# Performance work log

Measured on AMD Instinct MI355X. Metric: run time of the kernel, lower is better.

Reference implementation:

```python
import jax, jax.numpy as jnp
import numpy as np

B, N, C, K = 8, 4096, 128, 20  # batch, points-per-cloud, channels (n_cout), knn neighbors
NEG_SLOPE = 0.01  # torch F.leaky_relu default


def setup_inputs() -> dict:
    key = jax.random.key(0)
    ks = jax.random.split(key, 6)
    s = 1.0 / np.sqrt(C).astype(np.float32)
    xyz = jax.random.normal(ks[0], (B, 3, N), jnp.float32)
    points = jax.random.normal(ks[1], (B, C, N), jnp.float32)
    Wc = jax.random.normal(ks[2], (C, C), jnp.float32) * s  # center 1x1 conv weight (out,in)
    bc = jax.random.normal(ks[3], (C,), jnp.float32) * s
    Wg = jax.random.normal(ks[4], (C, C), jnp.float32) * s  # grouped 1x1 conv weight
    bg = jax.random.normal(ks[5], (C,), jnp.float32) * s
    return {"xyz": xyz, "points": points, "Wc": Wc, "bc": bc, "Wg": Wg, "bg": bg}


def reference(xyz, points, Wc, bc, Wg, bg):
    # xyz: [B,3,N], points: [B,C,N]
    k = K
    shortcut = points
    p = jax.nn.leaky_relu(points, NEG_SLOPE)        # [B,C,N]
    pt = jnp.transpose(p, (0, 2, 1))                # [B,N,C]
    xt = jnp.transpose(xyz, (0, 2, 1))              # [B,N,3]

    # pairwise squared distances [B,N,N]
    sq_norm = jnp.sum(xt * xt, axis=-1)             # [B,N]
    sq = sq_norm[:, :, None] - 2.0 * jnp.einsum('bnd,bmd->bnm', xt, xt) + sq_norm[:, None, :]

    # knn: k+1 nearest (incl. self), drop self -> [B,N,k]
    _, idx = jax.lax.top_k(-sq, k + 1)
    idx = idx[:, :, 1:]

    # gather neighbor features: [B,N,k,C]
    grouped = jax.vmap(lambda a, i: a[i])(pt, idx)

    # center 1x1 conv on [B,C,1,N] == per-point linear
    center = jnp.einsum('oc,bcn->bon', Wc, p) + bc[None, :, None]      # [B,C,N]
    # grouped 1x1 conv on [B,C,k,N]
    gout = jnp.einsum('oc,bnkc->bokn', Wg, grouped) + bg[None, :, None, None]  # [B,C,k,N]

    # mean over concat([center(1), grouped(k)], axis=2) then residual
    pooled = (center + jnp.sum(gout, axis=2)) / (k + 1)
    return pooled + shortcut
```

## Files before the change

kernel.cpp:

```cpp
#include <hip/hip_runtime.h>

#define B 8
#define N 4096
#define C 128
#define CL 128
#define KNN 21
#define CAP 22

typedef unsigned long long u64;
typedef unsigned int u32;
typedef unsigned short u16;

typedef __attribute__((ext_vector_type(8))) short bf16x8;
typedef __attribute__((ext_vector_type(4))) float f32x4;

__device__ __forceinline__ float bf2f(u16 u) {
    return __uint_as_float(((u32)u) << 16);
}
__device__ __forceinline__ u16 f2bf(float f) {
    u32 x = __float_as_uint(f);
    return (u16)((x + 0x7FFFu + ((x >> 16) & 1u)) >> 16);
}

__global__ __launch_bounds__(256) void k_transpose_lrelu(
        const float* __restrict__ pts, u16* __restrict__ X,
        const float* __restrict__ xyz, float4* __restrict__ cand) {
    __shared__ u16 tile[32][33];
    int b  = blockIdx.z;
    int c0 = blockIdx.y * 32;
    int n0 = blockIdx.x * 32;
    int tx = threadIdx.x, ty = threadIdx.y;

    if (blockIdx.y == 0 && ty == 0) {
        int n = n0 + tx;
        const float* xz = xyz + (size_t)b * 3 * N;
        float x = xz[n], y = xz[N + n], z = xz[2 * N + n];
        float sn = __fadd_rn(__fadd_rn(__fmul_rn(x, x), __fmul_rn(y, y)),
                             __fmul_rn(z, z));
        cand[(size_t)b * N + n] = make_float4(x, y, z, sn);
    }

    const float* src = pts + (size_t)b * C * N;
    #pragma unroll
    for (int i = 0; i < 32; i += 8) {
        float v = src[(size_t)(c0 + ty + i) * N + n0 + tx];
        if (v < 0.f) v = __fmul_rn(v, 0.01f);
        tile[ty + i][tx] = f2bf(v);
    }
    __syncthreads();
    u16* dst = X + (size_t)b * N * CL;
    #pragma unroll
    for (int i = 0; i < 32; i += 8) {
        dst[(size_t)(n0 + ty + i) * CL + (c0 + tx)] = tile[tx][ty + i];
    }
}

__global__ __launch_bounds__(256) void k_knn_gemm(
        const float4* __restrict__ cand, const u16* __restrict__ X,
        const float* __restrict__ Wc, const float* __restrict__ Wg,
        const float* __restrict__ pts, const float* __restrict__ bc,
        const float* __restrict__ bg, float* __restrict__ out) {
    __shared__ __align__(16) char lds[52224];
    float4* stg  = (float4*)lds;
    u32*    kbuf = (u32*)(lds + 18432);
    u16*    ibuf = (u16*)(lds + 18432 + 22528);
    u64*    mg   = (u64*)lds;
    u16 (*xs)[264] = (u16(*)[264])lds;
    __shared__ u16 win[64 * KNN];

    int tid = threadIdx.x;
    int w = tid >> 6, l = tid & 63;
    int b = blockIdx.y;
    int n0 = blockIdx.x * 64;
    int nq = n0 + l;

    const float4* candb = cand + (size_t)b * N;
    float4 cq = candb[nq];
    float qx = cq.x, qy = cq.y, qz = cq.z, snq = cq.w;

    u32 key[KNN], idx[KNN];
    #pragma unroll
    for (int i = 0; i < KNN; ++i) { key[i] = 0xFFFFFFFFu; idx[i] = 0u; }
    int cnt = 0;
    u32 thr = 0xFFFFFFFFu;

    auto compact = [&]() {
        #pragma unroll 1
        for (int i = 0; i < CAP; ++i) {
            if (__ballot(i < cnt) == 0ull) break;
            u32 kv = kbuf[i * 256 + tid];
            u32 iv = ibuf[i * 256 + tid];
            bool ins = (i < cnt) && (kv < key[20]);
            if (__ballot(ins) != 0ull) {
                key[20] = ins ? kv : key[20];
                idx[20] = ins ? iv : idx[20];
                #pragma unroll
                for (int t = 19; t >= 0; --t) {
                    bool sw = key[t] > key[t + 1];
                    u32 ka = sw ? key[t + 1] : key[t];
                    u32 kz = sw ? key[t] : key[t + 1];
                    u32 ia = sw ? idx[t + 1] : idx[t];
                    u32 iz = sw ? idx[t] : idx[t + 1];
                    key[t] = ka; key[t + 1] = kz;
                    idx[t] = ia; idx[t + 1] = iz;
                }
            }
        }
        cnt = 0;
        thr = key[20];
    };

    float4* mystg = stg + w * 288;
    int wl = l + (l >> 3);

    for (int sc = 0; sc < 4; ++sc) {
        int m0 = w * 1024 + sc * 256;
        float4 v0 = candb[m0 + l];
        float4 v1 = candb[m0 + l + 64];
        float4 v2 = candb[m0 + l + 128];
        float4 v3 = candb[m0 + l + 192];
        mystg[wl]       = v0;
        mystg[wl + 72]  = v1;
        mystg[wl + 144] = v2;
        mystg[wl + 216] = v3;
        asm volatile("s_waitcnt lgkmcnt(0)" ::: "memory");
        for (int cc = 0; cc < 256; cc += 8) {
            int base = cc + (cc >> 3);
            #pragma unroll
            for (int j = 0; j < 8; ++j) {
                float4 cp = mystg[base + j];
                int m = m0 + cc + j;
                float dot = __fadd_rn(__fadd_rn(__fmul_rn(qx, cp.x),
                                                __fmul_rn(qy, cp.y)),
                                      __fmul_rn(qz, cp.z));
                float sq = __fadd_rn(__fsub_rn(snq, __fadd_rn(dot, dot)), cp.w);
                u32 bits = __float_as_uint(sq);
                u32 kb = bits ^ (0x80000000u | (u32)(((int)bits) >> 31));
                kbuf[cnt * 256 + tid] = kb;
                ibuf[cnt * 256 + tid] = (u16)m;
                cnt += (kb < thr);
            }
            if (__ballot(cnt >= 15) != 0ull) compact();
        }
    }
    compact();

    __syncthreads();
    #pragma unroll
    for (int j = 0; j < KNN; ++j)
        mg[(w * 64 + l) * KNN + j] = ((u64)key[j] << 32) | (u64)idx[j];
    __syncthreads();

    if (w == 0) {
        int p0 = 0, p1 = 0, p2 = 0, p3 = 0;
        for (int j = 0; j < KNN; ++j) {
            u64 c0 = mg[(0 * 64 + l) * KNN + p0];
            u64 c1 = mg[(1 * 64 + l) * KNN + p1];
            u64 c2 = mg[(2 * 64 + l) * KNN + p2];
            u64 c3 = mg[(3 * 64 + l) * KNN + p3];
            u64 m01 = c0 < c1 ? c0 : c1; int s01 = c0 < c1 ? 0 : 1;
            u64 m23 = c2 < c3 ? c2 : c3; int s23 = c2 < c3 ? 2 : 3;
            u64 mm = m01 < m23 ? m01 : m23;
            int sel = m01 < m23 ? s01 : s23;
            win[l * KNN + j] = (u16)(mm & 0xFFFFu);
            p0 += (sel == 0); p1 += (sel == 1); p2 += (sel == 2); p3 += (sel == 3);
        }
    }
    __syncthreads();

    const u16* Xb = X + (size_t)b * N * CL;
    #pragma unroll
    for (int it = 0; it < 4; ++it) {
        int t = it * 256 + tid;
        int r = t >> 4, cch = t & 15;
        *(bf16x8*)(&xs[r][cch * 8]) =
            *(const bf16x8*)(Xb + (size_t)(n0 + r) * CL + cch * 8);
    }
    for (int qq = 0; qq < 16; ++qq) {
        int q = w * 16 + qq;
        float f0 = 0.f, f1 = 0.f;
        #pragma unroll
        for (int j = 1; j < KNN; ++j) {
            int m = win[q * KNN + j];
            u32 u2 = *(const u32*)(Xb + (size_t)m * CL + 2 * l);
            f0 += bf2f((u16)(u2 & 0xFFFFu));
            f1 += bf2f((u16)(u2 >> 16));
        }
        *(u32*)(&xs[q][128 + 2 * l]) =
            ((u32)f2bf(f1) << 16) | (u32)f2bf(f0);
    }
    __syncthreads();

    int lane = tid & 63;
    int l16 = lane & 15, lq = lane >> 4;
    const float* wc0 = Wc + (size_t)(w * 32 + l16) * 128 + lq * 8;
    const float* wc1 = Wc + (size_t)(w * 32 + 16 + l16) * 128 + lq * 8;
    const float* wg0 = Wg + (size_t)(w * 32 + l16) * 128 + lq * 8;
    const float* wg1 = Wg + (size_t)(w * 32 + 16 + l16) * 128 + lq * 8;

    f32x4 acc[2][4];
    #pragma unroll
    for (int oo = 0; oo < 2; ++oo)
        #pragma unroll
        for (int t = 0; t < 4; ++t)
            acc[oo][t] = (f32x4){0.f, 0.f, 0.f, 0.f};

    #pragma unroll
    for (int kk = 0; kk < 8; ++kk) {
        const float* s0 = (kk < 4) ? (wc0 + kk * 32) : (wg0 + (kk - 4) * 32);
        const float* s1 = (kk < 4) ? (wc1 + kk * 32) : (wg1 + (kk - 4) * 32);
        float4 wa0 = *(const float4*)s0, wb0 = *(const float4*)(s0 + 4);
        float4 wa1 = *(const float4*)s1, wb1 = *(const float4*)(s1 + 4);
        bf16x8 a0, a1;
        a0[0] = (short)f2bf(wa0.x); a0[1] = (short)f2bf(wa0.y);
        a0[2] = (short)f2bf(wa0.z); a0[3] = (short)f2bf(wa0.w);
        a0[4] = (short)f2bf(wb0.x); a0[5] = (short)f2bf(wb0.y);
        a0[6] = (short)f2bf(wb0.z); a0[7] = (short)f2bf(wb0.w);
        a1[0] = (short)f2bf(wa1.x); a1[1] = (short)f2bf(wa1.y);
        a1[2] = (short)f2bf(wa1.z); a1[3] = (short)f2bf(wa1.w);
        a1[4] = (short)f2bf(wb1.x); a1[5] = (short)f2bf(wb1.y);
        a1[6] = (short)f2bf(wb1.z); a1[7] = (short)f2bf(wb1.w);
        #pragma unroll
        for (int t = 0; t < 4; ++t) {
            bf16x8 bt = *(const bf16x8*)(&xs[t * 16 + l16][lq * 8 + kk * 32]);
            acc[0][t] = __builtin_amdgcn_mfma_f32_16x16x32_bf16(a0, bt,
                                                                acc[0][t], 0, 0, 0);
            acc[1][t] = __builtin_amdgcn_mfma_f32_16x16x32_bf16(a1, bt,
                                                                acc[1][t], 0, 0, 0);
        }
    }

    const float inv21 = 1.0f / 21.0f;
    const float* pb = pts + (size_t)b * C * N;
    float* ob = out + (size_t)b * C * N;
    #pragma unroll
    for (int oo = 0; oo < 2; ++oo) {
        float bias[4];
        #pragma unroll
        for (int r = 0; r < 4; ++r) {
            int o = w * 32 + oo * 16 + lq * 4 + r;
            bias[r] = bc[o] + 20.f * bg[o];
        }
        #pragma unroll
        for (int t = 0; t < 4; ++t) {
            int n = n0 + t * 16 + l16;
            #pragma unroll
            for (int r = 0; r < 4; ++r) {
                int o = w * 32 + oo * 16 + lq * 4 + r;
                ob[(size_t)o * N + n] =
                    (acc[oo][t][r] + bias[r]) * inv21 + pb[(size_t)o * N + n];
            }
        }
    }
}

extern "C" void kernel_launch(void* const* d_in, const int* in_sizes, int n_in,
                              void* d_out, int out_size, void* d_ws, size_t ws_size,
                              hipStream_t stream) {
    const float* xyz = (const float*)d_in[0];
    const float* pts = (const float*)d_in[1];
    const float* Wc  = (const float*)d_in[2];
    const float* bc  = (const float*)d_in[3];
    const float* Wg  = (const float*)d_in[4];
    const float* bg  = (const float*)d_in[5];
    float* out = (float*)d_out;

    u16* X = (u16*)d_ws;
    float4* cand = (float4*)((char*)d_ws +
                             (size_t)B * N * CL * sizeof(u16));

    k_transpose_lrelu<<<dim3(N / 32, C / 32, B), dim3(32, 8), 0, stream>>>(
        pts, X, xyz, cand);
    k_knn_gemm<<<dim3(N / 64, B), dim3(256), 0, stream>>>(
        cand, X, Wc, Wg, pts, bc, bg, out);
}
```

Baseline: 267.9 us.

## Fuse transpose/lrelu prep into main kNN-GEMM kernel via cooperative grid sync

Merges the separate transpose+leaky-relu+bf16 conversion kernel into the main kNN/GEMM kernel. Each block now converts its own 64-point tile through LDS with vectorized float4 loads and bf16x8 stores, then all blocks wait on a cooperative grid-wide sync before the neighbor search. The goal is to drop one kernel launch and the gap between the two kernels. In exchange it needs a cooperative launch with all 512 blocks resident at once, and it pays for a grid barrier.

```diff
diff --git a/kernel.cpp b/kernel.cpp
--- a/kernel.cpp
+++ b/kernel.cpp
@@ -1,4 +1,7 @@
 #include <hip/hip_runtime.h>
+#include <hip/hip_cooperative_groups.h>
+
+namespace cg = cooperative_groups;
 
 #define B 8
 #define N 4096
@@ -22,50 +25,19 @@
     return (u16)((x + 0x7FFFu + ((x >> 16) & 1u)) >> 16);
 }
 
-__global__ __launch_bounds__(256) void k_transpose_lrelu(
-        const float* __restrict__ pts, u16* __restrict__ X,
-        const float* __restrict__ xyz, float4* __restrict__ cand) {
-    __shared__ u16 tile[32][33];
-    int b  = blockIdx.z;
-    int c0 = blockIdx.y * 32;
-    int n0 = blockIdx.x * 32;
-    int tx = threadIdx.x, ty = threadIdx.y;
-
-    if (blockIdx.y == 0 && ty == 0) {
-        int n = n0 + tx;
-        const float* xz = xyz + (size_t)b * 3 * N;
-        float x = xz[n], y = xz[N + n], z = xz[2 * N + n];
-        float sn = __fadd_rn(__fadd_rn(__fmul_rn(x, x), __fmul_rn(y, y)),
-                             __fmul_rn(z, z));
-        cand[(size_t)b * N + n] = make_float4(x, y, z, sn);
-    }
-
-    const float* src = pts + (size_t)b * C * N;
-    #pragma unroll
-    for (int i = 0; i < 32; i += 8) {
-        float v = src[(size_t)(c0 + ty + i) * N + n0 + tx];
-        if (v < 0.f) v = __fmul_rn(v, 0.01f);
-        tile[ty + i][tx] = f2bf(v);
-    }
-    __syncthreads();
-    u16* dst = X + (size_t)b * N * CL;
-    #pragma unroll
-    for (int i = 0; i < 32; i += 8) {
-        dst[(size_t)(n0 + ty + i) * CL + (c0 + tx)] = tile[tx][ty + i];
-    }
-}
-
-__global__ __launch_bounds__(256) void k_knn_gemm(
-        const float4* __restrict__ cand, const u16* __restrict__ X,
+__global__ __launch_bounds__(256) void k_all(
+        float4* __restrict__ cand, u16* __restrict__ X,
         const float* __restrict__ Wc, const float* __restrict__ Wg,
         const float* __restrict__ pts, const float* __restrict__ bc,
-        const float* __restrict__ bg, float* __restrict__ out) {
+        const float* __restrict__ bg, float* __restrict__ out,
+        const float* __restrict__ xyz) {
     __shared__ __align__(16) char lds[52224];
     float4* stg  = (float4*)lds;
     u32*    kbuf = (u32*)(lds + 18432);
     u16*    ibuf = (u16*)(lds + 18432 + 22528);
     u64*    mg   = (u64*)lds;
     u16 (*xs)[264] = (u16(*)[264])lds;
+    u16 (*xt)[132] = (u16(*)[132])lds;
     __shared__ u16 win[64 * KNN];
 
     int tid = threadIdx.x;
@@ -73,6 +45,41 @@
     int b = blockIdx.y;
     int n0 = blockIdx.x * 64;
     int nq = n0 + l;
+
+    {
+        const float* src = pts + (size_t)b * C * N;
+        #pragma unroll
+        for (int it = 0; it < 8; ++it) {
+            int c  = it * 16 + (tid >> 4);
+            int j4 = (tid & 15) * 4;
+            float4 v = *(const float4*)(src + (size_t)c * N + n0 + j4);
+            float a0 = v.x, a1 = v.y, a2 = v.z, a3 = v.w;
+            if (a0 < 0.f) a0 = __fmul_rn(a0, 0.01f);
+            if (a1 < 0.f) a1 = __fmul_rn(a1, 0.01f);
+            if (a2 < 0.f) a2 = __fmul_rn(a2, 0.01f);
+            if (a3 < 0.f) a3 = __fmul_rn(a3, 0.01f);
+            xt[j4 + 0][c] = f2bf(a0);
+            xt[j4 + 1][c] = f2bf(a1);
+            xt[j4 + 2][c] = f2bf(a2);
+            xt[j4 + 3][c] = f2bf(a3);
+        }
+        if (tid < 64) {
+            int n = n0 + tid;
+            const float* xz = xyz + (size_t)b * 3 * N;
+            float x = xz[n], y = xz[N + n], z = xz[2 * N + n];
+            float sn = __fadd_rn(__fadd_rn(__fmul_rn(x, x), __fmul_rn(y, y)),
+                                 __fmul_rn(z, z));
+            cand[(size_t)b * N + n] = make_float4(x, y, z, sn);
+        }
+        __syncthreads();
+        int r = tid >> 2, qtr = tid & 3;
+        u16* Xrow = X + (size_t)(b * N + n0 + r) * CL + qtr * 32;
+        #pragma unroll
+        for (int s = 0; s < 4; ++s)
+            *(bf16x8*)(Xrow + s * 8) = *(const bf16x8*)(&xt[r][qtr * 32 + s * 8]);
+    }
+    __threadfence();
+    cg::this_grid().sync();
 
     const float4* candb = cand + (size_t)b * N;
     float4 cq = candb[nq];
@@ -269,8 +276,9 @@
     float4* cand = (float4*)((char*)d_ws +
                              (size_t)B * N * CL * sizeof(u16));
 
-    k_transpose_lrelu<<<dim3(N / 32, C / 32, B), dim3(32, 8), 0, stream>>>(
-        pts, X, xyz, cand);
-    k_knn_gemm<<<dim3(N / 64, B), dim3(256), 0, stream>>>(
-        cand, X, Wc, Wg, pts, bc, bg, out);
-}
+    void* args[] = {(void*)&cand, (void*)&X, (void*)&Wc, (void*)&Wg,
+                    (void*)&pts, (void*)&bc, (void*)&bg, (void*)&out,
+                    (void*)&xyz};
+    hipLaunchCooperativeKernel((void*)k_all, dim3(N / 64, B), dim3(256),
+                               args, 0, stream);
+}
```

Result: slower. 392.3 us (+46.4%).
